# Performance work log

Measured on AMD Instinct MI355X. Metric: run time of the kernel, lower is better.

Reference implementation:

```python
import jax, jax.numpy as jnp
import numpy as np

DELTA_VAR = 0.5
DELTA_DIST = 2.0
ALPHA = 1.0
BETA = 1.0
GAMMA = 0.001

N, E, D, H, W = 2, 16, 48, 160, 160
NUM_C = 32


def _safe_norm(x, axis):
    # L2 norm with zero-safe gradient (matches torch.norm 'fro' over the dim)
    d2 = jnp.sum(x * x, axis=axis)
    nz = d2 > 0
    return jnp.sqrt(jnp.where(nz, d2, 1.0)) * nz


def setup_inputs() -> dict:
    key = jax.random.key(0)
    k1, k2 = jax.random.split(key)
    input_ = jax.random.normal(k1, (N, E, D, H, W), dtype=jnp.float32)
    target = jax.random.randint(k2, (N, D, H, W), 0, NUM_C).astype(jnp.int64)
    return {"input_": input_, "target": target, "C": NUM_C}


def _single_loss(emb, labels, C):
    # emb: [E, V] flattened spatial; labels: [V] int in [0, C)
    V = labels.shape[0]
    counts = jax.ops.segment_sum(jnp.ones((V,), emb.dtype), labels, num_segments=C)  # [C]
    sums = jax.ops.segment_sum(emb.T, labels, num_segments=C)                         # [C, E]
    means = sums / counts[:, None]                                                     # [C, E]

    # variance term: per-voxel distance to own cluster mean (equivalent to the
    # one-hot-expanded CxExSPATIAL formulation after the target mask)
    dist = _safe_norm(emb.T - means[labels], axis=1)                                   # [V]
    hinge = jnp.maximum(dist - DELTA_VAR, 0.0) ** 2
    per_cluster = jax.ops.segment_sum(hinge, labels, num_segments=C) / counts          # [C]
    variance_term = jnp.sum(per_cluster) / C

    # distance term: pairwise cluster-mean repulsion
    diff = means[:, None, :] - means[None, :, :]                                       # [C, C, E]
    dmat = _safe_norm(diff, axis=2)                                                    # [C, C]
    repulsion = 2.0 * DELTA_DIST * (1.0 - jnp.eye(C, dtype=emb.dtype))
    hinged = jnp.maximum(repulsion - dmat, 0.0) ** 2
    distance_term = jnp.sum(hinged) / (C * (C - 1))

    # regularizer: mean L2 norm of cluster means
    regularizer_term = jnp.sum(_safe_norm(means, axis=1)) / C

    return ALPHA * variance_term + BETA * distance_term + GAMMA * regularizer_term


def reference(input_, target, C):
    n = input_.shape[0]
    emb = input_.reshape(n, input_.shape[1], -1)  # [N, E, V]
    lab = target.reshape(n, -1).astype(jnp.int32)  # [N, V]
    losses = jax.vmap(lambda e, l: _single_loss(e, l, C))(emb, lab)
    return jnp.sum(losses) / n
```

## Files before the change

kernel.cpp:

```cpp
#include <hip/hip_runtime.h>
#include <math.h>

constexpr int N_  = 2;
constexpr int E_  = 16;
constexpr int C_  = 32;
constexpr int V_  = 48 * 160 * 160;
constexpr int V4_ = V_ / 4;
constexpr int BLK = 256;

constexpr float DELTA_VAR  = 0.5f;
constexpr float DELTA_DIST = 2.0f;
constexpr float GAMMA      = 0.001f;

constexpr int NCOPY   = 8;
constexpr int WS_SUMT = 0;
constexpr int WS_CNT  = WS_SUMT + NCOPY * N_ * E_ * C_;
constexpr int WS_VAR  = WS_CNT  + NCOPY * N_ * C_;
constexpr int WS_FLOATS = WS_VAR + N_;

using short8 = __attribute__((ext_vector_type(8))) short;
using f32x4  = __attribute__((ext_vector_type(4))) float;

__device__ __forceinline__ unsigned short f2bf(float f) {
    unsigned u = __float_as_uint(f);
    return (unsigned short)((u + 0x7FFFu + ((u >> 16) & 1u)) >> 16);
}
__device__ __forceinline__ unsigned packlab(int4 t) {
    return (unsigned)t.x | ((unsigned)t.y << 8) | ((unsigned)t.z << 16) | ((unsigned)t.w << 24);
}

constexpr int XPAD = 520;
__global__ __launch_bounds__(BLK) void sums_mfma(
    const float4* __restrict__ x4, const int4* __restrict__ t4,
    float* __restrict__ ws)
{
    __shared__ unsigned short s_xb[2][E_ * XPAD];

    const int n     = blockIdx.y;
    const int gtile = blockIdx.x * 2048;
    const int tid   = threadIdx.x;
    const int lane  = tid & 63;
    const int wid   = tid >> 6;
    const int myc   = lane & 15;
    const int quad  = lane >> 4;

    const short one = 0x3F80;
    short8 A_ones = {one, one, one, one, one, one, one, one};

    f32x4 acc_lo = {0.f,0.f,0.f,0.f}, acc_hi = {0.f,0.f,0.f,0.f};
    f32x4 cnt_lo = {0.f,0.f,0.f,0.f}, cnt_hi = {0.f,0.f,0.f,0.f};

    float4 R[8];
    {
        const int tb4 = gtile >> 2;
        #pragma unroll
        for (int k = 0; k < 8; ++k) {
            const int i = k * BLK + tid, e = i >> 7, v4 = i & 127;
            R[k] = x4[((size_t)(n * E_ + e)) * V4_ + tb4 + v4];
        }
    }

    for (int t = 0; t < 4; ++t) {
        const int tbase4 = (gtile + t * 512) >> 2;
        unsigned short* buf = s_xb[t & 1];

        #pragma unroll
        for (int k = 0; k < 8; ++k) {
            const int i = k * BLK + tid, e = i >> 7, v4 = i & 127;
            uint2 p;
            p.x = (unsigned)f2bf(R[k].x) | ((unsigned)f2bf(R[k].y) << 16);
            p.y = (unsigned)f2bf(R[k].z) | ((unsigned)f2bf(R[k].w) << 16);
            *(uint2*)&buf[e * XPAD + v4 * 4] = p;
        }
        if (t < 3) {
            const int nb4 = (gtile + (t + 1) * 512) >> 2;
            #pragma unroll
            for (int k = 0; k < 8; ++k) {
                const int i = k * BLK + tid, e = i >> 7, v4 = i & 127;
                R[k] = x4[((size_t)(n * E_ + e)) * V4_ + nb4 + v4];
            }
        }
        const int wbase = wid * 128;
        int4 P[4], Q[4];
        #pragma unroll
        for (int s = 0; s < 4; ++s) {
            const int b4 = tbase4 + ((wbase + s * 32 + quad * 8) >> 2);
            P[s] = t4[(size_t)n * V4_ + b4];
            Q[s] = t4[(size_t)n * V4_ + b4 + 1];
        }

        __builtin_amdgcn_sched_barrier(0);
        asm volatile("s_waitcnt lgkmcnt(0)");
        __builtin_amdgcn_s_barrier();
        __builtin_amdgcn_sched_barrier(0);

        #pragma unroll
        for (int s = 0; s < 4; ++s) {
            const int lvb = wbase + s * 32;
            const short8 A = *(const short8*)&buf[myc * XPAD + lvb + quad * 8];
            const unsigned la = packlab(P[s]), lb2 = packlab(Q[s]);
            short8 Blo, Bhi;
            #pragma unroll
            for (int j = 0; j < 4; ++j) {
                const int c0 = (la  >> (8 * j)) & 255;
                const int c1 = (lb2 >> (8 * j)) & 255;
                Blo[j]     = (c0 == myc)      ? one : (short)0;
                Bhi[j]     = (c0 == myc + 16) ? one : (short)0;
                Blo[4 + j] = (c1 == myc)      ? one : (short)0;
                Bhi[4 + j] = (c1 == myc + 16) ? one : (short)0;
            }
            acc_lo = __builtin_amdgcn_mfma_f32_16x16x32_bf16(A, Blo, acc_lo, 0, 0, 0);
            acc_hi = __builtin_amdgcn_mfma_f32_16x16x32_bf16(A, Bhi, acc_hi, 0, 0, 0);
            cnt_lo = __builtin_amdgcn_mfma_f32_16x16x32_bf16(A_ones, Blo, cnt_lo, 0, 0, 0);
            cnt_hi = __builtin_amdgcn_mfma_f32_16x16x32_bf16(A_ones, Bhi, cnt_hi, 0, 0, 0);
        }
    }

    float* s_red = (float*)&s_xb[0][0];
    #pragma unroll
    for (int r = 0; r < 4; ++r) {
        s_red[wid * 512 + lane * 8 + r]     = acc_lo[r];
        s_red[wid * 512 + lane * 8 + 4 + r] = acc_hi[r];
    }
    if (quad == 0) {
        s_red[2048 + wid * 32 + myc]      = cnt_lo[0];
        s_red[2048 + wid * 32 + myc + 16] = cnt_hi[0];
    }
    __syncthreads();

    const int kc = blockIdx.x & (NCOPY - 1);
    float* gsumT = ws + WS_SUMT + kc * (N_ * E_ * C_);
    float* gcntk = ws + WS_CNT  + kc * (N_ * C_);
    #pragma unroll
    for (int u = 0; u < 2; ++u) {
        const int combo = tid * 2 + u;
        const int l = combo >> 3, k = combo & 7;
        const int e = (l >> 4) * 4 + (k & 3);
        const int c = (l & 15) + 16 * (k >> 2);
        const float v = s_red[combo] + s_red[512 + combo]
                      + s_red[1024 + combo] + s_red[1536 + combo];
        unsafeAtomicAdd(&gsumT[(n * E_ + e) * C_ + c], v);
    }
    if (tid < C_) {
        const float v = s_red[2048 + tid] + s_red[2048 + 32 + tid]
                      + s_red[2048 + 64 + tid] + s_red[2048 + 96 + tid];
        unsafeAtomicAdd(&gcntk[n * C_ + tid], v);
    }
}

constexpr int MUP = 20;
__global__ __launch_bounds__(BLK) void variance_f32(
    const float4* __restrict__ x4, const int4* __restrict__ t4,
    float* __restrict__ ws)
{
    __shared__ float s_mu[C_ * MUP];
    __shared__ float s_part[4];
    const float* gsumT = ws + WS_SUMT;
    const float* gcnt  = ws + WS_CNT;
    float*       gvar  = ws + WS_VAR;

    const int n = blockIdx.y, tid = threadIdx.x;
    const int v4g = blockIdx.x * BLK + tid;

    const int4 t = t4[(size_t)n * V4_ + v4g];
    const float4* xrow = x4 + (size_t)n * E_ * V4_ + v4g;
    float4 xs[16];
    #pragma unroll
    for (int e = 0; e < 16; ++e) xs[e] = xrow[(size_t)e * V4_];

    for (int i = tid; i < C_ * E_; i += BLK) {
        const int c = i >> 4, e = i & 15;
        float s = 0.f, cc = 0.f;
        #pragma unroll
        for (int k = 0; k < NCOPY; ++k) {
            s  += gsumT[k * (N_ * E_ * C_) + (n * E_ + e) * C_ + c];
            cc += gcnt [k * (N_ * C_) + n * C_ + c];
        }
        s_mu[c * MUP + e] = s / cc;
        if (e == 0) s_mu[c * MUP + 16] = 1.0f / (cc * (float)C_);
    }
    __syncthreads();

    const int l0 = t.x, l1 = t.y, l2 = t.z, l3 = t.w;
    float4 m0[4], m1[4], m2[4], m3[4];
    #pragma unroll
    for (int u = 0; u < 4; ++u) {
        m0[u] = *(const float4*)&s_mu[l0 * MUP + 4 * u];
        m1[u] = *(const float4*)&s_mu[l1 * MUP + 4 * u];
        m2[u] = *(const float4*)&s_mu[l2 * MUP + 4 * u];
        m3[u] = *(const float4*)&s_mu[l3 * MUP + 4 * u];
    }
    const float w0 = s_mu[l0 * MUP + 16], w1 = s_mu[l1 * MUP + 16];
    const float w2 = s_mu[l2 * MUP + 16], w3 = s_mu[l3 * MUP + 16];

    float d0 = 0.f, d1 = 0.f, d2 = 0.f, d3 = 0.f;
    #pragma unroll
    for (int e = 0; e < 16; ++e) {
        const float mu0 = ((const float*)&m0[e >> 2])[e & 3];
        const float mu1 = ((const float*)&m1[e >> 2])[e & 3];
        const float mu2 = ((const float*)&m2[e >> 2])[e & 3];
        const float mu3 = ((const float*)&m3[e >> 2])[e & 3];
        d0 += (xs[e].x - mu0) * (xs[e].x - mu0);
        d1 += (xs[e].y - mu1) * (xs[e].y - mu1);
        d2 += (xs[e].z - mu2) * (xs[e].z - mu2);
        d3 += (xs[e].w - mu3) * (xs[e].w - mu3);
    }
    const float h0 = fmaxf(sqrtf(d0) - DELTA_VAR, 0.f);
    const float h1 = fmaxf(sqrtf(d1) - DELTA_VAR, 0.f);
    const float h2 = fmaxf(sqrtf(d2) - DELTA_VAR, 0.f);
    const float h3 = fmaxf(sqrtf(d3) - DELTA_VAR, 0.f);
    float v = h0 * h0 * w0 + h1 * h1 * w1 + h2 * h2 * w2 + h3 * h3 * w3;

    #pragma unroll
    for (int off = 32; off > 0; off >>= 1)
        v += __shfl_down(v, off, 64);
    if ((tid & 63) == 0) s_part[tid >> 6] = v;
    __syncthreads();
    if (tid == 0)
        unsafeAtomicAdd(&gvar[n], s_part[0] + s_part[1] + s_part[2] + s_part[3]);
}

__global__ __launch_bounds__(BLK) void finalize(
    const float* __restrict__ ws, float* __restrict__ out)
{
    __shared__ float s_mean[C_ * 17];
    __shared__ float s_red;
    __shared__ float s_total;

    const float* gsumT = ws + WS_SUMT;
    const float* gcnt  = ws + WS_CNT;
    const float* gvar  = ws + WS_VAR;

    if (threadIdx.x == 0) s_total = 0.0f;

    for (int n = 0; n < N_; ++n) {
        __syncthreads();
        for (int i = threadIdx.x; i < C_ * E_; i += BLK) {
            const int c = i >> 4, e = i & 15;
            float s = 0.f, cc = 0.f;
            #pragma unroll
            for (int k = 0; k < NCOPY; ++k) {
                s  += gsumT[k * (N_ * E_ * C_) + (n * E_ + e) * C_ + c];
                cc += gcnt [k * (N_ * C_) + n * C_ + c];
            }
            s_mean[c * 17 + e] = s / cc;
        }
        if (threadIdx.x == 0) s_red = gvar[n];
        __syncthreads();

        float local = 0.0f;
        if (threadIdx.x < C_) {
            const int c = threadIdx.x;
            float d2 = 0.f;
            #pragma unroll
            for (int e = 0; e < E_; ++e) {
                const float m = s_mean[c * 17 + e];
                d2 += m * m;
            }
            const float nm = d2 > 0.f ? sqrtf(d2) : 0.f;
            local += GAMMA * nm / (float)C_;
        }
        for (int t = threadIdx.x; t < C_ * C_; t += BLK) {
            const int i = t >> 5, j = t & 31;
            if (i != j) {
                float d2 = 0.f;
                #pragma unroll
                for (int e = 0; e < E_; ++e) {
                    const float diff = s_mean[i * 17 + e] - s_mean[j * 17 + e];
                    d2 += diff * diff;
                }
                const float d = d2 > 0.f ? sqrtf(d2) : 0.f;
                const float h = fmaxf(2.0f * DELTA_DIST - d, 0.f);
                local += (h * h) / (float)(C_ * (C_ - 1));
            }
        }
        unsafeAtomicAdd(&s_red, local);
        __syncthreads();
        if (threadIdx.x == 0) s_total += s_red;
    }
    __syncthreads();
    if (threadIdx.x == 0) out[0] = s_total / (float)N_;
}

extern "C" void kernel_launch(void* const* d_in, const int* in_sizes, int n_in,
                              void* d_out, int out_size, void* d_ws, size_t ws_size,
                              hipStream_t stream) {
    const float4* x4 = (const float4*)d_in[0];
    const int4*   t4 = (const int4*)d_in[1];
    float* ws  = (float*)d_ws;
    float* out = (float*)d_out;

    hipMemsetAsync(d_ws, 0, WS_FLOATS * sizeof(float), stream);

    sums_mfma   <<<dim3(600, N_),        BLK, 0, stream>>>(x4, t4, ws);
    variance_f32<<<dim3(V4_ / BLK, N_),  BLK, 0, stream>>>(x4, t4, ws);
    finalize    <<<1, BLK, 0, stream>>>(ws, out);
}
```

Baseline: 285.8 us.

## Fuse sums, variance and finalize into one cooperative persistent kernel

Replaces the three launches with a single cooperative kernel of 768 persistent blocks that runs the sums, variance and finalize phases separated by grid-wide syncs. The sums phase drops the LDS staging: each wave loads its embedding and label vectors straight into registers through a three-deep prefetch ring and feeds them to the MFMA. The variance phase becomes grid-stride over both batches and spreads its atomics across copies. The aim is to remove launch gaps and LDS round-trips, at the cost of grid-sync overhead, lower occupancy, and a fallback to separate kernels if the cooperative launch fails.

Result: slower. 456.5 us (+59.7%).

```diff
diff --git a/kernel.cpp b/kernel.cpp
--- a/kernel.cpp
+++ b/kernel.cpp
@@ -1,5 +1,8 @@
 #include <hip/hip_runtime.h>
+#include <hip/hip_cooperative_groups.h>
 #include <math.h>
+
+namespace cg = cooperative_groups;
 
 constexpr int N_  = 2;
 constexpr int E_  = 16;
@@ -8,15 +11,23 @@
 constexpr int V4_ = V_ / 4;
 constexpr int BLK = 256;
 
+constexpr int G_     = 768;
+constexpr int HALF_  = G_ / 2;
+constexpr int WPB_   = HALF_ * 4;
+constexpr int VPW_   = V_ / WPB_;
+constexpr int NSTEP_ = VPW_ / 32;
+
 constexpr float DELTA_VAR  = 0.5f;
 constexpr float DELTA_DIST = 2.0f;
 constexpr float GAMMA      = 0.001f;
 
-constexpr int NCOPY   = 8;
-constexpr int WS_SUMT = 0;
-constexpr int WS_CNT  = WS_SUMT + NCOPY * N_ * E_ * C_;
-constexpr int WS_VAR  = WS_CNT  + NCOPY * N_ * C_;
-constexpr int WS_FLOATS = WS_VAR + N_;
+constexpr int NCOPY     = 8;
+constexpr int WS_SUMT   = 0;
+constexpr int WS_CNT    = WS_SUMT + NCOPY * N_ * E_ * C_;
+constexpr int WS_VAR    = WS_CNT  + NCOPY * N_ * C_;
+constexpr int WS_FLOATS = WS_VAR  + NCOPY * N_;
+
+constexpr int MUP = 20;
 
 using short8 = __attribute__((ext_vector_type(8))) short;
 using f32x4  = __attribute__((ext_vector_type(4))) float;
@@ -29,94 +40,72 @@
     return (unsigned)t.x | ((unsigned)t.y << 8) | ((unsigned)t.z << 16) | ((unsigned)t.w << 24);
 }
 
-constexpr int XPAD = 520;
-__global__ __launch_bounds__(BLK) void sums_mfma(
-    const float4* __restrict__ x4, const int4* __restrict__ t4,
-    float* __restrict__ ws)
-{
-    __shared__ unsigned short s_xb[2][E_ * XPAD];
-
-    const int n     = blockIdx.y;
-    const int gtile = blockIdx.x * 2048;
-    const int tid   = threadIdx.x;
-    const int lane  = tid & 63;
-    const int wid   = tid >> 6;
-    const int myc   = lane & 15;
-    const int quad  = lane >> 4;
-
-    const short one = 0x3F80;
+__device__ __forceinline__ void phase_sums(
+    const float4* __restrict__ x4, const int4* __restrict__ t4,
+    float* __restrict__ ws, float* s_red, int bid)
+{
+    const int tid  = threadIdx.x;
+    const int lane = tid & 63;
+    const int wid  = tid >> 6;
+    const int myc  = lane & 15;
+    const int quad = lane >> 4;
+
+    const int n  = bid / HALF_;
+    const int wb = (bid % HALF_) * 4 + wid;
+    const float4* __restrict__ xrow = x4 + (size_t)(n * E_ + myc) * V4_;
+    const int4*   __restrict__ t4n  = t4 + (size_t)n * V4_;
+    const int l4 = wb * (VPW_ / 4) + quad * 2;
+
+    const short one = (short)0x3F80;
     short8 A_ones = {one, one, one, one, one, one, one, one};
 
     f32x4 acc_lo = {0.f,0.f,0.f,0.f}, acc_hi = {0.f,0.f,0.f,0.f};
     f32x4 cnt_lo = {0.f,0.f,0.f,0.f}, cnt_hi = {0.f,0.f,0.f,0.f};
 
-    float4 R[8];
-    {
-        const int tb4 = gtile >> 2;
-        #pragma unroll
-        for (int k = 0; k < 8; ++k) {
-            const int i = k * BLK + tid, e = i >> 7, v4 = i & 127;
-            R[k] = x4[((size_t)(n * E_ + e)) * V4_ + tb4 + v4];
-        }
-    }
-
-    for (int t = 0; t < 4; ++t) {
-        const int tbase4 = (gtile + t * 512) >> 2;
-        unsigned short* buf = s_xb[t & 1];
-
-        #pragma unroll
-        for (int k = 0; k < 8; ++k) {
-            const int i = k * BLK + tid, e = i >> 7, v4 = i & 127;
-            uint2 p;
-            p.x = (unsigned)f2bf(R[k].x) | ((unsigned)f2bf(R[k].y) << 16);
-            p.y = (unsigned)f2bf(R[k].z) | ((unsigned)f2bf(R[k].w) << 16);
-            *(uint2*)&buf[e * XPAD + v4 * 4] = p;
-        }
-        if (t < 3) {
-            const int nb4 = (gtile + (t + 1) * 512) >> 2;
-            #pragma unroll
-            for (int k = 0; k < 8; ++k) {
-                const int i = k * BLK + tid, e = i >> 7, v4 = i & 127;
-                R[k] = x4[((size_t)(n * E_ + e)) * V4_ + nb4 + v4];
-            }
-        }
-        const int wbase = wid * 128;
-        int4 P[4], Q[4];
-        #pragma unroll
-        for (int s = 0; s < 4; ++s) {
-            const int b4 = tbase4 + ((wbase + s * 32 + quad * 8) >> 2);
-            P[s] = t4[(size_t)n * V4_ + b4];
-            Q[s] = t4[(size_t)n * V4_ + b4 + 1];
-        }
-
-        __builtin_amdgcn_sched_barrier(0);
-        asm volatile("s_waitcnt lgkmcnt(0)");
-        __builtin_amdgcn_s_barrier();
-        __builtin_amdgcn_sched_barrier(0);
-
-        #pragma unroll
-        for (int s = 0; s < 4; ++s) {
-            const int lvb = wbase + s * 32;
-            const short8 A = *(const short8*)&buf[myc * XPAD + lvb + quad * 8];
-            const unsigned la = packlab(P[s]), lb2 = packlab(Q[s]);
-            short8 Blo, Bhi;
-            #pragma unroll
-            for (int j = 0; j < 4; ++j) {
-                const int c0 = (la  >> (8 * j)) & 255;
-                const int c1 = (lb2 >> (8 * j)) & 255;
-                Blo[j]     = (c0 == myc)      ? one : (short)0;
-                Bhi[j]     = (c0 == myc + 16) ? one : (short)0;
-                Blo[4 + j] = (c1 == myc)      ? one : (short)0;
-                Bhi[4 + j] = (c1 == myc + 16) ? one : (short)0;
-            }
-            acc_lo = __builtin_amdgcn_mfma_f32_16x16x32_bf16(A, Blo, acc_lo, 0, 0, 0);
-            acc_hi = __builtin_amdgcn_mfma_f32_16x16x32_bf16(A, Bhi, acc_hi, 0, 0, 0);
-            cnt_lo = __builtin_amdgcn_mfma_f32_16x16x32_bf16(A_ones, Blo, cnt_lo, 0, 0, 0);
-            cnt_hi = __builtin_amdgcn_mfma_f32_16x16x32_bf16(A_ones, Bhi, cnt_hi, 0, 0, 0);
-        }
-    }
-
-    float* s_red = (float*)&s_xb[0][0];
+    float4 RX0[3], RX1[3];
+    int4   RP[3],  RQ[3];
+    #pragma unroll
+    for (int p = 0; p < 2; ++p) {
+        RX0[p] = xrow[l4 + p * 8];
+        RX1[p] = xrow[l4 + p * 8 + 1];
+        RP[p]  = t4n[l4 + p * 8];
+        RQ[p]  = t4n[l4 + p * 8 + 1];
+    }
+
+    #pragma unroll
+    for (int s = 0; s < NSTEP_; ++s) {
+        const int cur = s % 3;
+        if (s + 2 < NSTEP_) {
+            const int nxt = (s + 2) % 3;
+            RX0[nxt] = xrow[l4 + (s + 2) * 8];
+            RX1[nxt] = xrow[l4 + (s + 2) * 8 + 1];
+            RP[nxt]  = t4n[l4 + (s + 2) * 8];
+            RQ[nxt]  = t4n[l4 + (s + 2) * 8 + 1];
+        }
+        short8 A;
+        A[0] = (short)f2bf(RX0[cur].x); A[1] = (short)f2bf(RX0[cur].y);
+        A[2] = (short)f2bf(RX0[cur].z); A[3] = (short)f2bf(RX0[cur].w);
+        A[4] = (short)f2bf(RX1[cur].x); A[5] = (short)f2bf(RX1[cur].y);
+        A[6] = (short)f2bf(RX1[cur].z); A[7] = (short)f2bf(RX1[cur].w);
+
+        const unsigned la  = packlab(RP[cur]);
+        const unsigned lb2 = packlab(RQ[cur]);
+        short8 Blo, Bhi;
+        #pragma unroll
+        for (int j = 0; j < 4; ++j) {
+            const int c0 = (la  >> (8 * j)) & 255;
+            const int c1 = (lb2 >> (8 * j)) & 255;
+            Blo[j]     = (c0 == myc)      ? one : (short)0;
+            Bhi[j]     = (c0 == myc + 16) ? one : (short)0;
+            Blo[4 + j] = (c1 == myc)      ? one : (short)0;
+            Bhi[4 + j] = (c1 == myc + 16) ? one : (short)0;
+        }
+        acc_lo = __builtin_amdgcn_mfma_f32_16x16x32_bf16(A,      Blo, acc_lo, 0, 0, 0);
+        acc_hi = __builtin_amdgcn_mfma_f32_16x16x32_bf16(A,      Bhi, acc_hi, 0, 0, 0);
+        cnt_lo = __builtin_amdgcn_mfma_f32_16x16x32_bf16(A_ones, Blo, cnt_lo, 0, 0, 0);
+        cnt_hi = __builtin_amdgcn_mfma_f32_16x16x32_bf16(A_ones, Bhi, cnt_hi, 0, 0, 0);
+    }
+
     #pragma unroll
     for (int r = 0; r < 4; ++r) {
         s_red[wid * 512 + lane * 8 + r]     = acc_lo[r];
@@ -128,7 +117,7 @@
     }
     __syncthreads();
 
-    const int kc = blockIdx.x & (NCOPY - 1);
+    const int kc = bid & (NCOPY - 1);
     float* gsumT = ws + WS_SUMT + kc * (N_ * E_ * C_);
     float* gcntk = ws + WS_CNT  + kc * (N_ * C_);
     #pragma unroll
@@ -148,90 +137,102 @@
     }
 }
 
-constexpr int MUP = 20;
-__global__ __launch_bounds__(BLK) void variance_f32(
-    const float4* __restrict__ x4, const int4* __restrict__ t4,
-    float* __restrict__ ws)
-{
-    __shared__ float s_mu[C_ * MUP];
-    __shared__ float s_part[4];
+__device__ __forceinline__ void phase_var(
+    const float4* __restrict__ x4, const int4* __restrict__ t4,
+    float* __restrict__ ws, float* s_mu, int bid, int nblk)
+{
     const float* gsumT = ws + WS_SUMT;
     const float* gcnt  = ws + WS_CNT;
     float*       gvar  = ws + WS_VAR;
-
-    const int n = blockIdx.y, tid = threadIdx.x;
-    const int v4g = blockIdx.x * BLK + tid;
-
-    const int4 t = t4[(size_t)n * V4_ + v4g];
-    const float4* xrow = x4 + (size_t)n * E_ * V4_ + v4g;
-    float4 xs[16];
-    #pragma unroll
-    for (int e = 0; e < 16; ++e) xs[e] = xrow[(size_t)e * V4_];
-
-    for (int i = tid; i < C_ * E_; i += BLK) {
-        const int c = i >> 4, e = i & 15;
+    const int tid = threadIdx.x;
+
+    for (int i = tid; i < N_ * C_ * E_; i += BLK) {
+        const int n2 = i >> 9;
+        const int r  = i & 511;
+        const int c  = r >> 4, e = r & 15;
         float s = 0.f, cc = 0.f;
         #pragma unroll
         for (int k = 0; k < NCOPY; ++k) {
-            s  += gsumT[k * (N_ * E_ * C_) + (n * E_ + e) * C_ + c];
-            cc += gcnt [k * (N_ * C_) + n * C_ + c];
-        }
-        s_mu[c * MUP + e] = s / cc;
-        if (e == 0) s_mu[c * MUP + 16] = 1.0f / (cc * (float)C_);
+            s  += gsumT[k * (N_ * E_ * C_) + (n2 * E_ + e) * C_ + c];
+            cc += gcnt [k * (N_ * C_) + n2 * C_ + c];
+        }
+        s_mu[n2 * (C_ * MUP) + c * MUP + e] = s / cc;
+        if (e == 0) s_mu[n2 * (C_ * MUP) + c * MUP + 16] = 1.0f / (cc * (float)C_);
     }
     __syncthreads();
 
-    const int l0 = t.x, l1 = t.y, l2 = t.z, l3 = t.w;
-    float4 m0[4], m1[4], m2[4], m3[4];
-    #pragma unroll
-    for (int u = 0; u < 4; ++u) {
-        m0[u] = *(const float4*)&s_mu[l0 * MUP + 4 * u];
-        m1[u] = *(const float4*)&s_mu[l1 * MUP + 4 * u];
-        m2[u] = *(const float4*)&s_mu[l2 * MUP + 4 * u];
-        m3[u] = *(const float4*)&s_mu[l3 * MUP + 4 * u];
-    }
-    const float w0 = s_mu[l0 * MUP + 16], w1 = s_mu[l1 * MUP + 16];
-    const float w2 = s_mu[l2 * MUP + 16], w3 = s_mu[l3 * MUP + 16];
-
-    float d0 = 0.f, d1 = 0.f, d2 = 0.f, d3 = 0.f;
-    #pragma unroll
-    for (int e = 0; e < 16; ++e) {
-        const float mu0 = ((const float*)&m0[e >> 2])[e & 3];
-        const float mu1 = ((const float*)&m1[e >> 2])[e & 3];
-        const float mu2 = ((const float*)&m2[e >> 2])[e & 3];
-        const float mu3 = ((const float*)&m3[e >> 2])[e & 3];
-        d0 += (xs[e].x - mu0) * (xs[e].x - mu0);
-        d1 += (xs[e].y - mu1) * (xs[e].y - mu1);
-        d2 += (xs[e].z - mu2) * (xs[e].z - mu2);
-        d3 += (xs[e].w - mu3) * (xs[e].w - mu3);
-    }
-    const float h0 = fmaxf(sqrtf(d0) - DELTA_VAR, 0.f);
-    const float h1 = fmaxf(sqrtf(d1) - DELTA_VAR, 0.f);
-    const float h2 = fmaxf(sqrtf(d2) - DELTA_VAR, 0.f);
-    const float h3 = fmaxf(sqrtf(d3) - DELTA_VAR, 0.f);
-    float v = h0 * h0 * w0 + h1 * h1 * w1 + h2 * h2 * w2 + h3 * h3 * w3;
-
-    #pragma unroll
-    for (int off = 32; off > 0; off >>= 1)
-        v += __shfl_down(v, off, 64);
-    if ((tid & 63) == 0) s_part[tid >> 6] = v;
+    float va0 = 0.f, va1 = 0.f;
+    for (int g = bid * BLK + tid; g < N_ * V4_; g += nblk * BLK) {
+        const int n  = (g >= V4_) ? 1 : 0;
+        const int vg = g - n * V4_;
+        const int4 t = t4[g];
+        const float4* __restrict__ xr = x4 + (size_t)n * E_ * V4_ + vg;
+        float4 xs[16];
+        #pragma unroll
+        for (int e = 0; e < 16; ++e) xs[e] = xr[(size_t)e * V4_];
+
+        const float* mu = s_mu + n * (C_ * MUP);
+        const int l0 = t.x, l1 = t.y, l2 = t.z, l3 = t.w;
+        float4 m0[4], m1[4], m2[4], m3[4];
+        #pragma unroll
+        for (int u = 0; u < 4; ++u) {
+            m0[u] = *(const float4*)&mu[l0 * MUP + 4 * u];
+            m1[u] = *(const float4*)&mu[l1 * MUP + 4 * u];
+            m2[u] = *(const float4*)&mu[l2 * MUP + 4 * u];
+            m3[u] = *(const float4*)&mu[l3 * MUP + 4 * u];
+        }
+        const float w0 = mu[l0 * MUP + 16], w1 = mu[l1 * MUP + 16];
+        const float w2 = mu[l2 * MUP + 16], w3 = mu[l3 * MUP + 16];
+
+        float d0 = 0.f, d1 = 0.f, d2 = 0.f, d3 = 0.f;
+        #pragma unroll
+        for (int e = 0; e < 16; ++e) {
+            const float mu0 = ((const float*)&m0[e >> 2])[e & 3];
+            const float mu1 = ((const float*)&m1[e >> 2])[e & 3];
+            const float mu2 = ((const float*)&m2[e >> 2])[e & 3];
+            const float mu3 = ((const float*)&m3[e >> 2])[e & 3];
+            d0 += (xs[e].x - mu0) * (xs[e].x - mu0);
+            d1 += (xs[e].y - mu1) * (xs[e].y - mu1);
+            d2 += (xs[e].z - mu2) * (xs[e].z - mu2);
+            d3 += (xs[e].w - mu3) * (xs[e].w - mu3);
+        }
+        const float h0 = fmaxf(sqrtf(d0) - DELTA_VAR, 0.f);
+        const float h1 = fmaxf(sqrtf(d1) - DELTA_VAR, 0.f);
+        const float h2 = fmaxf(sqrtf(d2) - DELTA_VAR, 0.f);
+        const float h3 = fmaxf(sqrtf(d3) - DELTA_VAR, 0.f);
+        const float vv = h0 * h0 * w0 + h1 * h1 * w1 + h2 * h2 * w2 + h3 * h3 * w3;
+        va0 += (n == 0) ? vv : 0.f;
+        va1 += (n == 0) ? 0.f : vv;
+    }
+
+    #pragma unroll
+    for (int off = 32; off > 0; off >>= 1) {
+        va0 += __shfl_down(va0, off, 64);
+        va1 += __shfl_down(va1, off, 64);
+    }
+    const int base = N_ * C_ * MUP;
+    if ((tid & 63) == 0) {
+        s_mu[base + (tid >> 6) * 2]     = va0;
+        s_mu[base + (tid >> 6) * 2 + 1] = va1;
+    }
     __syncthreads();
-    if (tid == 0)
-        unsafeAtomicAdd(&gvar[n], s_part[0] + s_part[1] + s_part[2] + s_part[3]);
-}
-
-__global__ __launch_bounds__(BLK) void finalize(
-    const float* __restrict__ ws, float* __restrict__ out)
-{
-    __shared__ float s_mean[C_ * 17];
-    __shared__ float s_red;
-    __shared__ float s_total;
-
+    if (tid == 0) {
+        const float t0 = s_mu[base] + s_mu[base + 2] + s_mu[base + 4] + s_mu[base + 6];
+        const float t1 = s_mu[base + 1] + s_mu[base + 3] + s_mu[base + 5] + s_mu[base + 7];
+        const int kc = bid & (NCOPY - 1);
+        unsafeAtomicAdd(&gvar[kc * N_ + 0], t0);
+        unsafeAtomicAdd(&gvar[kc * N_ + 1], t1);
+    }
+}
+
+__device__ __forceinline__ void phase_fin(
+    const float* __restrict__ ws, float* __restrict__ out, float* sm)
+{
     const float* gsumT = ws + WS_SUMT;
     const float* gcnt  = ws + WS_CNT;
     const float* gvar  = ws + WS_VAR;
 
-    if (threadIdx.x == 0) s_total = 0.0f;
+    if (threadIdx.x == 0) sm[601] = 0.0f;
 
     for (int n = 0; n < N_; ++n) {
         __syncthreads();
@@ -243,9 +244,14 @@
                 s  += gsumT[k * (N_ * E_ * C_) + (n * E_ + e) * C_ + c];
                 cc += gcnt [k * (N_ * C_) + n * C_ + c];
             }
-            s_mean[c * 17 + e] = s / cc;
-        }
-        if (threadIdx.x == 0) s_red = gvar[n];
+            sm[c * 17 + e] = s / cc;
+        }
+        if (threadIdx.x == 0) {
+            float vs = 0.f;
+            #pragma unroll
+            for (int k = 0; k < NCOPY; ++k) vs += gvar[k * N_ + n];
+            sm[600] = vs;
+        }
         __syncthreads();
 
         float local = 0.0f;
@@ -254,7 +260,7 @@
             float d2 = 0.f;
             #pragma unroll
             for (int e = 0; e < E_; ++e) {
-                const float m = s_mean[c * 17 + e];
+                const float m = sm[c * 17 + e];
                 d2 += m * m;
             }
             const float nm = d2 > 0.f ? sqrtf(d2) : 0.f;
@@ -266,7 +272,7 @@
                 float d2 = 0.f;
                 #pragma unroll
                 for (int e = 0; e < E_; ++e) {
-                    const float diff = s_mean[i * 17 + e] - s_mean[j * 17 + e];
+                    const float diff = sm[i * 17 + e] - sm[j * 17 + e];
                     d2 += diff * diff;
                 }
                 const float d = d2 > 0.f ? sqrtf(d2) : 0.f;
@@ -274,12 +280,50 @@
                 local += (h * h) / (float)(C_ * (C_ - 1));
             }
         }
-        unsafeAtomicAdd(&s_red, local);
+        unsafeAtomicAdd(&sm[600], local);
         __syncthreads();
-        if (threadIdx.x == 0) s_total += s_red;
+        if (threadIdx.x == 0) sm[601] += sm[600];
     }
     __syncthreads();
-    if (threadIdx.x == 0) out[0] = s_total / (float)N_;
+    if (threadIdx.x == 0) out[0] = sm[601] / (float)N_;
+}
+
+__global__ __launch_bounds__(BLK, 3) void fused_all(
+    const float4* __restrict__ x4, const int4* __restrict__ t4,
+    float* __restrict__ ws, float* __restrict__ out)
+{
+    __shared__ float s_red[2176];
+    __shared__ float s_mu[N_ * C_ * MUP + 16];
+    const int bid = blockIdx.x;
+
+    phase_sums(x4, t4, ws, s_red, bid);
+    cg::this_grid().sync();
+    phase_var(x4, t4, ws, s_mu, bid, (int)gridDim.x);
+    cg::this_grid().sync();
+    if (bid == 0) phase_fin(ws, out, s_mu);
+}
+
+__global__ __launch_bounds__(BLK, 3) void k_sums(
+    const float4* __restrict__ x4, const int4* __restrict__ t4,
+    float* __restrict__ ws)
+{
+    __shared__ float s_red[2176];
+    phase_sums(x4, t4, ws, s_red, blockIdx.x);
+}
+
+__global__ __launch_bounds__(BLK, 3) void k_var(
+    const float4* __restrict__ x4, const int4* __restrict__ t4,
+    float* __restrict__ ws)
+{
+    __shared__ float s_mu[N_ * C_ * MUP + 16];
+    phase_var(x4, t4, ws, s_mu, blockIdx.x, (int)gridDim.x);
+}
+
+__global__ __launch_bounds__(BLK) void k_fin(
+    const float* __restrict__ ws, float* __restrict__ out)
+{
+    __shared__ float sm[N_ * C_ * MUP + 16];
+    phase_fin(ws, out, sm);
 }
 
 extern "C" void kernel_launch(void* const* d_in, const int* in_sizes, int n_in,
@@ -292,7 +336,13 @@
 
     hipMemsetAsync(d_ws, 0, WS_FLOATS * sizeof(float), stream);
 
-    sums_mfma   <<<dim3(600, N_),        BLK, 0, stream>>>(x4, t4, ws);
-    variance_f32<<<dim3(V4_ / BLK, N_),  BLK, 0, stream>>>(x4, t4, ws);
-    finalize    <<<1, BLK, 0, stream>>>(ws, out);
-}
+    void* args[] = {(void*)&x4, (void*)&t4, (void*)&ws, (void*)&out};
+    hipError_t err = hipLaunchCooperativeKernel(
+        (const void*)fused_all, dim3(G_), dim3(BLK), args, 0, stream);
+    if (err != hipSuccess) {
+        (void)hipGetLastError();
+        k_sums<<<dim3(G_), BLK, 0, stream>>>(x4, t4, ws);
+        k_var <<<dim3(G_), BLK, 0, stream>>>(x4, t4, ws);
+        k_fin <<<1,        BLK, 0, stream>>>(ws, out);
+    }
+}
```

## Fold mean and finalize stages into last-block tickets, use persistent grids

Applied to the files above, without the earlier changes.

Removes the separate finalize launch by having the last block of each kernel (detected via an atomic ticket counter) compute the cluster means or the final loss. Means are computed once into workspace instead of being re-reduced in every variance block. Both kernels switch to fixed 1024-block grid-stride layouts with interleaved batch handling and occupancy hints. The cost is a serialized tail in the last block plus extra fences and atomics.

Result: slower. 443.7 us (+55.2%).

```diff
diff --git a/kernel.cpp b/kernel.cpp
--- a/kernel.cpp
+++ b/kernel.cpp
@@ -8,15 +8,25 @@
 constexpr int V4_ = V_ / 4;
 constexpr int BLK = 256;
 
+constexpr int TILE = 512;
+constexpr int TPN_ = V_ / TILE;
+constexpr int GS   = 1024;
+constexpr int SPB_ = GS / N_;
+constexpr int GV   = 1024;
+
 constexpr float DELTA_VAR  = 0.5f;
 constexpr float DELTA_DIST = 2.0f;
 constexpr float GAMMA      = 0.001f;
 
-constexpr int NCOPY   = 8;
-constexpr int WS_SUMT = 0;
-constexpr int WS_CNT  = WS_SUMT + NCOPY * N_ * E_ * C_;
-constexpr int WS_VAR  = WS_CNT  + NCOPY * N_ * C_;
-constexpr int WS_FLOATS = WS_VAR + N_;
+constexpr int NCOPY     = 8;
+constexpr int MUP       = 20;
+constexpr int WS_SUMT   = 0;
+constexpr int WS_CNT    = WS_SUMT + NCOPY * N_ * E_ * C_;
+constexpr int WS_VAR    = WS_CNT  + NCOPY * N_ * C_;
+constexpr int WS_TK1    = WS_VAR  + NCOPY * N_;
+constexpr int WS_TK2    = WS_TK1 + 1;
+constexpr int WS_MU     = 8728;
+constexpr int WS_FLOATS = WS_MU + N_ * C_ * MUP;
 
 using short8 = __attribute__((ext_vector_type(8))) short;
 using f32x4  = __attribute__((ext_vector_type(4))) float;
@@ -28,23 +38,33 @@
 __device__ __forceinline__ unsigned packlab(int4 t) {
     return (unsigned)t.x | ((unsigned)t.y << 8) | ((unsigned)t.z << 16) | ((unsigned)t.w << 24);
 }
+__device__ __forceinline__ float gload(const float* p) {
+    return __hip_atomic_load(p, __ATOMIC_RELAXED, __HIP_MEMORY_SCOPE_AGENT);
+}
 
 constexpr int XPAD = 520;
-__global__ __launch_bounds__(BLK) void sums_mfma(
+__global__ __launch_bounds__(BLK, 4) void k_sums(
     const float4* __restrict__ x4, const int4* __restrict__ t4,
     float* __restrict__ ws)
 {
     __shared__ unsigned short s_xb[2][E_ * XPAD];
-
-    const int n     = blockIdx.y;
-    const int gtile = blockIdx.x * 2048;
-    const int tid   = threadIdx.x;
-    const int lane  = tid & 63;
-    const int wid   = tid >> 6;
-    const int myc   = lane & 15;
-    const int quad  = lane >> 4;
-
-    const short one = 0x3F80;
+    __shared__ unsigned s_flag;
+
+    const int b    = blockIdx.x;
+    const int tid  = threadIdx.x;
+    const int lane = tid & 63;
+    const int wid  = tid >> 6;
+    const int myc  = lane & 15;
+    const int quad = lane >> 4;
+
+    const int n  = b & 1;
+    const int bs = b >> 1;
+    const int nt = (bs < (TPN_ - 4 * SPB_)) ? 5 : 4;
+
+    const float4* __restrict__ xn  = x4 + (size_t)(n * E_) * V4_;
+    const int4*   __restrict__ t4n = t4 + (size_t)n * V4_;
+
+    const short one = (short)0x3F80;
     short8 A_ones = {one, one, one, one, one, one, one, one};
 
     f32x4 acc_lo = {0.f,0.f,0.f,0.f}, acc_hi = {0.f,0.f,0.f,0.f};
@@ -52,17 +72,17 @@
 
     float4 R[8];
     {
-        const int tb4 = gtile >> 2;
+        const int tb4 = bs * (TILE / 4);
         #pragma unroll
         for (int k = 0; k < 8; ++k) {
             const int i = k * BLK + tid, e = i >> 7, v4 = i & 127;
-            R[k] = x4[((size_t)(n * E_ + e)) * V4_ + tb4 + v4];
-        }
-    }
-
-    for (int t = 0; t < 4; ++t) {
-        const int tbase4 = (gtile + t * 512) >> 2;
-        unsigned short* buf = s_xb[t & 1];
+            R[k] = xn[(size_t)e * V4_ + tb4 + v4];
+        }
+    }
+
+    for (int it = 0; it < nt; ++it) {
+        const int tbase4 = (bs + it * SPB_) * (TILE / 4);
+        unsigned short* buf = s_xb[it & 1];
 
         #pragma unroll
         for (int k = 0; k < 8; ++k) {
@@ -72,12 +92,12 @@
             p.y = (unsigned)f2bf(R[k].z) | ((unsigned)f2bf(R[k].w) << 16);
             *(uint2*)&buf[e * XPAD + v4 * 4] = p;
         }
-        if (t < 3) {
-            const int nb4 = (gtile + (t + 1) * 512) >> 2;
+        if (it + 1 < nt) {
+            const int nb4 = (bs + (it + 1) * SPB_) * (TILE / 4);
             #pragma unroll
             for (int k = 0; k < 8; ++k) {
                 const int i = k * BLK + tid, e = i >> 7, v4 = i & 127;
-                R[k] = x4[((size_t)(n * E_ + e)) * V4_ + nb4 + v4];
+                R[k] = xn[(size_t)e * V4_ + nb4 + v4];
             }
         }
         const int wbase = wid * 128;
@@ -85,8 +105,8 @@
         #pragma unroll
         for (int s = 0; s < 4; ++s) {
             const int b4 = tbase4 + ((wbase + s * 32 + quad * 8) >> 2);
-            P[s] = t4[(size_t)n * V4_ + b4];
-            Q[s] = t4[(size_t)n * V4_ + b4 + 1];
+            P[s] = t4n[b4];
+            Q[s] = t4n[b4 + 1];
         }
 
         __builtin_amdgcn_sched_barrier(0);
@@ -109,13 +129,14 @@
                 Blo[4 + j] = (c1 == myc)      ? one : (short)0;
                 Bhi[4 + j] = (c1 == myc + 16) ? one : (short)0;
             }
-            acc_lo = __builtin_amdgcn_mfma_f32_16x16x32_bf16(A, Blo, acc_lo, 0, 0, 0);
-            acc_hi = __builtin_amdgcn_mfma_f32_16x16x32_bf16(A, Bhi, acc_hi, 0, 0, 0);
+            acc_lo = __builtin_amdgcn_mfma_f32_16x16x32_bf16(A,      Blo, acc_lo, 0, 0, 0);
+            acc_hi = __builtin_amdgcn_mfma_f32_16x16x32_bf16(A,      Bhi, acc_hi, 0, 0, 0);
             cnt_lo = __builtin_amdgcn_mfma_f32_16x16x32_bf16(A_ones, Blo, cnt_lo, 0, 0, 0);
             cnt_hi = __builtin_amdgcn_mfma_f32_16x16x32_bf16(A_ones, Bhi, cnt_hi, 0, 0, 0);
         }
     }
 
+    __syncthreads();
     float* s_red = (float*)&s_xb[0][0];
     #pragma unroll
     for (int r = 0; r < 4; ++r) {
@@ -128,7 +149,7 @@
     }
     __syncthreads();
 
-    const int kc = blockIdx.x & (NCOPY - 1);
+    const int kc = bs & (NCOPY - 1);
     float* gsumT = ws + WS_SUMT + kc * (N_ * E_ * C_);
     float* gcntk = ws + WS_CNT  + kc * (N_ * C_);
     #pragma unroll
@@ -146,140 +167,151 @@
                       + s_red[2048 + 64 + tid] + s_red[2048 + 96 + tid];
         unsafeAtomicAdd(&gcntk[n * C_ + tid], v);
     }
-}
-
-constexpr int MUP = 20;
-__global__ __launch_bounds__(BLK) void variance_f32(
-    const float4* __restrict__ x4, const int4* __restrict__ t4,
-    float* __restrict__ ws)
-{
-    __shared__ float s_mu[C_ * MUP];
-    __shared__ float s_part[4];
-    const float* gsumT = ws + WS_SUMT;
-    const float* gcnt  = ws + WS_CNT;
-    float*       gvar  = ws + WS_VAR;
-
-    const int n = blockIdx.y, tid = threadIdx.x;
-    const int v4g = blockIdx.x * BLK + tid;
-
-    const int4 t = t4[(size_t)n * V4_ + v4g];
-    const float4* xrow = x4 + (size_t)n * E_ * V4_ + v4g;
-    float4 xs[16];
-    #pragma unroll
-    for (int e = 0; e < 16; ++e) xs[e] = xrow[(size_t)e * V4_];
-
-    for (int i = tid; i < C_ * E_; i += BLK) {
-        const int c = i >> 4, e = i & 15;
-        float s = 0.f, cc = 0.f;
-        #pragma unroll
-        for (int k = 0; k < NCOPY; ++k) {
-            s  += gsumT[k * (N_ * E_ * C_) + (n * E_ + e) * C_ + c];
-            cc += gcnt [k * (N_ * C_) + n * C_ + c];
-        }
-        s_mu[c * MUP + e] = s / cc;
-        if (e == 0) s_mu[c * MUP + 16] = 1.0f / (cc * (float)C_);
-    }
-    __syncthreads();
-
-    const int l0 = t.x, l1 = t.y, l2 = t.z, l3 = t.w;
-    float4 m0[4], m1[4], m2[4], m3[4];
-    #pragma unroll
-    for (int u = 0; u < 4; ++u) {
-        m0[u] = *(const float4*)&s_mu[l0 * MUP + 4 * u];
-        m1[u] = *(const float4*)&s_mu[l1 * MUP + 4 * u];
-        m2[u] = *(const float4*)&s_mu[l2 * MUP + 4 * u];
-        m3[u] = *(const float4*)&s_mu[l3 * MUP + 4 * u];
-    }
-    const float w0 = s_mu[l0 * MUP + 16], w1 = s_mu[l1 * MUP + 16];
-    const float w2 = s_mu[l2 * MUP + 16], w3 = s_mu[l3 * MUP + 16];
-
-    float d0 = 0.f, d1 = 0.f, d2 = 0.f, d3 = 0.f;
-    #pragma unroll
-    for (int e = 0; e < 16; ++e) {
-        const float mu0 = ((const float*)&m0[e >> 2])[e & 3];
-        const float mu1 = ((const float*)&m1[e >> 2])[e & 3];
-        const float mu2 = ((const float*)&m2[e >> 2])[e & 3];
-        const float mu3 = ((const float*)&m3[e >> 2])[e & 3];
-        d0 += (xs[e].x - mu0) * (xs[e].x - mu0);
-        d1 += (xs[e].y - mu1) * (xs[e].y - mu1);
-        d2 += (xs[e].z - mu2) * (xs[e].z - mu2);
-        d3 += (xs[e].w - mu3) * (xs[e].w - mu3);
-    }
-    const float h0 = fmaxf(sqrtf(d0) - DELTA_VAR, 0.f);
-    const float h1 = fmaxf(sqrtf(d1) - DELTA_VAR, 0.f);
-    const float h2 = fmaxf(sqrtf(d2) - DELTA_VAR, 0.f);
-    const float h3 = fmaxf(sqrtf(d3) - DELTA_VAR, 0.f);
-    float v = h0 * h0 * w0 + h1 * h1 * w1 + h2 * h2 * w2 + h3 * h3 * w3;
-
-    #pragma unroll
-    for (int off = 32; off > 0; off >>= 1)
-        v += __shfl_down(v, off, 64);
-    if ((tid & 63) == 0) s_part[tid >> 6] = v;
-    __syncthreads();
-    if (tid == 0)
-        unsafeAtomicAdd(&gvar[n], s_part[0] + s_part[1] + s_part[2] + s_part[3]);
-}
-
-__global__ __launch_bounds__(BLK) void finalize(
-    const float* __restrict__ ws, float* __restrict__ out)
-{
-    __shared__ float s_mean[C_ * 17];
-    __shared__ float s_red;
-    __shared__ float s_total;
-
-    const float* gsumT = ws + WS_SUMT;
-    const float* gcnt  = ws + WS_CNT;
-    const float* gvar  = ws + WS_VAR;
-
-    if (threadIdx.x == 0) s_total = 0.0f;
-
-    for (int n = 0; n < N_; ++n) {
-        __syncthreads();
-        for (int i = threadIdx.x; i < C_ * E_; i += BLK) {
-            const int c = i >> 4, e = i & 15;
+
+    __threadfence();
+    __syncthreads();
+    if (tid == 0) {
+        unsigned* tk = (unsigned*)(ws + WS_TK1);
+        s_flag = (atomicAdd(tk, 1u) == (unsigned)(GS - 1)) ? 1u : 0u;
+    }
+    __syncthreads();
+    if (s_flag) {
+        __threadfence();
+        const float* gS = ws + WS_SUMT;
+        const float* gC = ws + WS_CNT;
+        float*       mu = ws + WS_MU;
+        for (int i = tid; i < N_ * C_ * E_; i += BLK) {
+            const int n2 = i >> 9;
+            const int r  = i & 511;
+            const int c  = r >> 4, e = r & 15;
             float s = 0.f, cc = 0.f;
             #pragma unroll
             for (int k = 0; k < NCOPY; ++k) {
-                s  += gsumT[k * (N_ * E_ * C_) + (n * E_ + e) * C_ + c];
-                cc += gcnt [k * (N_ * C_) + n * C_ + c];
-            }
-            s_mean[c * 17 + e] = s / cc;
-        }
-        if (threadIdx.x == 0) s_red = gvar[n];
-        __syncthreads();
-
-        float local = 0.0f;
-        if (threadIdx.x < C_) {
-            const int c = threadIdx.x;
-            float d2 = 0.f;
-            #pragma unroll
-            for (int e = 0; e < E_; ++e) {
-                const float m = s_mean[c * 17 + e];
-                d2 += m * m;
-            }
-            const float nm = d2 > 0.f ? sqrtf(d2) : 0.f;
-            local += GAMMA * nm / (float)C_;
-        }
-        for (int t = threadIdx.x; t < C_ * C_; t += BLK) {
-            const int i = t >> 5, j = t & 31;
-            if (i != j) {
+                s  += gload(&gS[k * (N_ * E_ * C_) + (n2 * E_ + e) * C_ + c]);
+                cc += gload(&gC[k * (N_ * C_) + n2 * C_ + c]);
+            }
+            mu[(n2 * C_ + c) * MUP + e] = s / cc;
+            if (e == 0) mu[(n2 * C_ + c) * MUP + 16] = 1.0f / (cc * (float)C_);
+        }
+    }
+}
+
+__global__ __launch_bounds__(BLK, 4) void k_var(
+    const float4* __restrict__ x4, const int4* __restrict__ t4,
+    float* __restrict__ ws, float* __restrict__ out)
+{
+    __shared__ float s_mu[N_ * C_ * MUP];
+    __shared__ float s_aux[8];
+    __shared__ unsigned s_flag;
+
+    float* gvar = ws + WS_VAR;
+    const int bid = blockIdx.x, tid = threadIdx.x;
+    const int lane = tid & 63, wid = tid >> 6;
+
+    {
+        const float* mu = ws + WS_MU;
+        for (int i = tid; i < N_ * C_ * MUP; i += BLK) s_mu[i] = mu[i];
+    }
+    __syncthreads();
+
+    float va0 = 0.f, va1 = 0.f;
+    for (int g = bid * BLK + tid; g < N_ * V4_; g += GV * BLK) {
+        const int n  = (g >= V4_) ? 1 : 0;
+        const int vg = g - n * V4_;
+        const int4 t = t4[g];
+        const float4* __restrict__ xr = x4 + (size_t)n * E_ * V4_ + vg;
+        float4 xs[16];
+        #pragma unroll
+        for (int e = 0; e < 16; ++e) xs[e] = xr[(size_t)e * V4_];
+
+        const int mb = n * (C_ * MUP);
+        const int b0 = mb + t.x * MUP, b1 = mb + t.y * MUP;
+        const int b2 = mb + t.z * MUP, b3 = mb + t.w * MUP;
+        const float w0 = s_mu[b0 + 16], w1 = s_mu[b1 + 16];
+        const float w2 = s_mu[b2 + 16], w3 = s_mu[b3 + 16];
+
+        float d0 = 0.f, d1 = 0.f, d2 = 0.f, d3 = 0.f;
+        #pragma unroll
+        for (int e = 0; e < 16; ++e) {
+            const float mu0 = s_mu[b0 + e];
+            const float mu1 = s_mu[b1 + e];
+            const float mu2 = s_mu[b2 + e];
+            const float mu3 = s_mu[b3 + e];
+            d0 += (xs[e].x - mu0) * (xs[e].x - mu0);
+            d1 += (xs[e].y - mu1) * (xs[e].y - mu1);
+            d2 += (xs[e].z - mu2) * (xs[e].z - mu2);
+            d3 += (xs[e].w - mu3) * (xs[e].w - mu3);
+        }
+        const float h0 = fmaxf(sqrtf(d0) - DELTA_VAR, 0.f);
+        const float h1 = fmaxf(sqrtf(d1) - DELTA_VAR, 0.f);
+        const float h2 = fmaxf(sqrtf(d2) - DELTA_VAR, 0.f);
+        const float h3 = fmaxf(sqrtf(d3) - DELTA_VAR, 0.f);
+        const float vv = h0 * h0 * w0 + h1 * h1 * w1 + h2 * h2 * w2 + h3 * h3 * w3;
+        va0 += (n == 0) ? vv : 0.f;
+        va1 += (n == 0) ? 0.f : vv;
+    }
+
+    #pragma unroll
+    for (int off = 32; off > 0; off >>= 1) {
+        va0 += __shfl_down(va0, off, 64);
+        va1 += __shfl_down(va1, off, 64);
+    }
+    if (lane == 0) { s_aux[wid * 2] = va0; s_aux[wid * 2 + 1] = va1; }
+    __syncthreads();
+    if (tid == 0) {
+        const float t0 = s_aux[0] + s_aux[2] + s_aux[4] + s_aux[6];
+        const float t1 = s_aux[1] + s_aux[3] + s_aux[5] + s_aux[7];
+        const int kc = bid & (NCOPY - 1);
+        unsafeAtomicAdd(&gvar[kc * N_ + 0], t0);
+        unsafeAtomicAdd(&gvar[kc * N_ + 1], t1);
+        __threadfence();
+        unsigned* tk = (unsigned*)(ws + WS_TK2);
+        s_flag = (atomicAdd(tk, 1u) == (unsigned)(GV - 1)) ? 1u : 0u;
+    }
+    __syncthreads();
+
+    if (s_flag) {
+        __threadfence();
+        float local = 0.f;
+        if (tid < NCOPY * N_) local += gload(&gvar[tid]);
+
+        for (int n = 0; n < N_; ++n) {
+            const float* mu = s_mu + n * (C_ * MUP);
+            if (tid < C_) {
+                const int c = tid;
                 float d2 = 0.f;
                 #pragma unroll
                 for (int e = 0; e < E_; ++e) {
-                    const float diff = s_mean[i * 17 + e] - s_mean[j * 17 + e];
-                    d2 += diff * diff;
+                    const float m = mu[c * MUP + e];
+                    d2 += m * m;
                 }
-                const float d = d2 > 0.f ? sqrtf(d2) : 0.f;
-                const float h = fmaxf(2.0f * DELTA_DIST - d, 0.f);
-                local += (h * h) / (float)(C_ * (C_ - 1));
-            }
-        }
-        unsafeAtomicAdd(&s_red, local);
+                const float nm = d2 > 0.f ? sqrtf(d2) : 0.f;
+                local += GAMMA * nm / (float)C_;
+            }
+            for (int t2 = tid; t2 < C_ * C_; t2 += BLK) {
+                const int i = t2 >> 5, j = t2 & 31;
+                if (i != j) {
+                    float d2 = 0.f;
+                    #pragma unroll
+                    for (int e = 0; e < E_; ++e) {
+                        const float diff = mu[i * MUP + e] - mu[j * MUP + e];
+                        d2 += diff * diff;
+                    }
+                    const float d = d2 > 0.f ? sqrtf(d2) : 0.f;
+                    const float h = fmaxf(2.0f * DELTA_DIST - d, 0.f);
+                    local += (h * h) / (float)(C_ * (C_ - 1));
+                }
+            }
+        }
+
+        #pragma unroll
+        for (int off = 32; off > 0; off >>= 1)
+            local += __shfl_down(local, off, 64);
+        if (lane == 0) s_aux[wid] = local;
         __syncthreads();
-        if (threadIdx.x == 0) s_total += s_red;
-    }
-    __syncthreads();
-    if (threadIdx.x == 0) out[0] = s_total / (float)N_;
+        if (tid == 0)
+            out[0] = (s_aux[0] + s_aux[1] + s_aux[2] + s_aux[3]) / (float)N_;
+    }
 }
 
 extern "C" void kernel_launch(void* const* d_in, const int* in_sizes, int n_in,
@@ -292,7 +324,6 @@
 
     hipMemsetAsync(d_ws, 0, WS_FLOATS * sizeof(float), stream);
 
-    sums_mfma   <<<dim3(600, N_),        BLK, 0, stream>>>(x4, t4, ws);
-    variance_f32<<<dim3(V4_ / BLK, N_),  BLK, 0, stream>>>(x4, t4, ws);
-    finalize    <<<1, BLK, 0, stream>>>(ws, out);
-}
+    k_sums<<<dim3(GS), BLK, 0, stream>>>(x4, t4, ws);
+    k_var <<<dim3(GV), BLK, 0, stream>>>(x4, t4, ws, out);
+}
```

## Fuse finalize into variance kernel via last-block ticket and spread variance atomics

Applied to the files above, without the earlier changes.

The separate finalize launch is removed. The last variance block to finish, found with an atomic ticket counter and threadfences, now computes the distance and regularizer terms and writes the output. The variance partial sums are spread over 8 copies to cut atomic contention on a single address. The label loads in the sums kernel move ahead of the next-tile prefetch, and the tile loop is unrolled. This saves one kernel launch and its tail, at the cost of a serialized finalize step inside the last block and extra atomics.

After: 348.6 us. 1.22x slower.

```diff
diff --git a/kernel.cpp b/kernel.cpp
--- a/kernel.cpp
+++ b/kernel.cpp
@@ -12,11 +12,15 @@
 constexpr float DELTA_DIST = 2.0f;
 constexpr float GAMMA      = 0.001f;
 
-constexpr int NCOPY   = 8;
-constexpr int WS_SUMT = 0;
-constexpr int WS_CNT  = WS_SUMT + NCOPY * N_ * E_ * C_;
-constexpr int WS_VAR  = WS_CNT  + NCOPY * N_ * C_;
-constexpr int WS_FLOATS = WS_VAR + N_;
+constexpr int NCOPY     = 8;
+constexpr int WS_SUMT   = 0;
+constexpr int WS_CNT    = WS_SUMT + NCOPY * N_ * E_ * C_;
+constexpr int WS_VAR    = WS_CNT  + NCOPY * N_ * C_;
+constexpr int WS_TK     = WS_VAR  + NCOPY * N_;
+constexpr int WS_FLOATS = WS_TK + 4;
+
+constexpr int MUP = 20;
+constexpr int GVB = 1200 * N_;
 
 using short8 = __attribute__((ext_vector_type(8))) short;
 using f32x4  = __attribute__((ext_vector_type(4))) float;
@@ -27,6 +31,9 @@
 }
 __device__ __forceinline__ unsigned packlab(int4 t) {
     return (unsigned)t.x | ((unsigned)t.y << 8) | ((unsigned)t.z << 16) | ((unsigned)t.w << 24);
+}
+__device__ __forceinline__ float gload(const float* p) {
+    return __hip_atomic_load(p, __ATOMIC_RELAXED, __HIP_MEMORY_SCOPE_AGENT);
 }
 
 constexpr int XPAD = 520;
@@ -44,7 +51,7 @@
     const int myc   = lane & 15;
     const int quad  = lane >> 4;
 
-    const short one = 0x3F80;
+    const short one = (short)0x3F80;
     short8 A_ones = {one, one, one, one, one, one, one, one};
 
     f32x4 acc_lo = {0.f,0.f,0.f,0.f}, acc_hi = {0.f,0.f,0.f,0.f};
@@ -60,6 +67,7 @@
         }
     }
 
+    #pragma unroll
     for (int t = 0; t < 4; ++t) {
         const int tbase4 = (gtile + t * 512) >> 2;
         unsigned short* buf = s_xb[t & 1];
@@ -72,6 +80,14 @@
             p.y = (unsigned)f2bf(R[k].z) | ((unsigned)f2bf(R[k].w) << 16);
             *(uint2*)&buf[e * XPAD + v4 * 4] = p;
         }
+        const int wbase = wid * 128;
+        int4 P[4], Q[4];
+        #pragma unroll
+        for (int s = 0; s < 4; ++s) {
+            const int b4 = tbase4 + ((wbase + s * 32 + quad * 8) >> 2);
+            P[s] = t4[(size_t)n * V4_ + b4];
+            Q[s] = t4[(size_t)n * V4_ + b4 + 1];
+        }
         if (t < 3) {
             const int nb4 = (gtile + (t + 1) * 512) >> 2;
             #pragma unroll
@@ -79,14 +95,6 @@
                 const int i = k * BLK + tid, e = i >> 7, v4 = i & 127;
                 R[k] = x4[((size_t)(n * E_ + e)) * V4_ + nb4 + v4];
             }
-        }
-        const int wbase = wid * 128;
-        int4 P[4], Q[4];
-        #pragma unroll
-        for (int s = 0; s < 4; ++s) {
-            const int b4 = tbase4 + ((wbase + s * 32 + quad * 8) >> 2);
-            P[s] = t4[(size_t)n * V4_ + b4];
-            Q[s] = t4[(size_t)n * V4_ + b4 + 1];
         }
 
         __builtin_amdgcn_sched_barrier(0);
@@ -109,8 +117,8 @@
                 Blo[4 + j] = (c1 == myc)      ? one : (short)0;
                 Bhi[4 + j] = (c1 == myc + 16) ? one : (short)0;
             }
-            acc_lo = __builtin_amdgcn_mfma_f32_16x16x32_bf16(A, Blo, acc_lo, 0, 0, 0);
-            acc_hi = __builtin_amdgcn_mfma_f32_16x16x32_bf16(A, Bhi, acc_hi, 0, 0, 0);
+            acc_lo = __builtin_amdgcn_mfma_f32_16x16x32_bf16(A,      Blo, acc_lo, 0, 0, 0);
+            acc_hi = __builtin_amdgcn_mfma_f32_16x16x32_bf16(A,      Bhi, acc_hi, 0, 0, 0);
             cnt_lo = __builtin_amdgcn_mfma_f32_16x16x32_bf16(A_ones, Blo, cnt_lo, 0, 0, 0);
             cnt_hi = __builtin_amdgcn_mfma_f32_16x16x32_bf16(A_ones, Bhi, cnt_hi, 0, 0, 0);
         }
@@ -148,13 +156,16 @@
     }
 }
 
-constexpr int MUP = 20;
 __global__ __launch_bounds__(BLK) void variance_f32(
     const float4* __restrict__ x4, const int4* __restrict__ t4,
-    float* __restrict__ ws)
+    float* __restrict__ ws, float* __restrict__ out)
 {
     __shared__ float s_mu[C_ * MUP];
     __shared__ float s_part[4];
+    __shared__ float s_mean[C_ * 17];
+    __shared__ float s_red2, s_total;
+    __shared__ unsigned s_flag;
+
     const float* gsumT = ws + WS_SUMT;
     const float* gcnt  = ws + WS_CNT;
     float*       gvar  = ws + WS_VAR;
@@ -163,7 +174,7 @@
     const int v4g = blockIdx.x * BLK + tid;
 
     const int4 t = t4[(size_t)n * V4_ + v4g];
-    const float4* xrow = x4 + (size_t)n * E_ * V4_ + v4g;
+    const float4* __restrict__ xrow = x4 + (size_t)n * E_ * V4_ + v4g;
     float4 xs[16];
     #pragma unroll
     for (int e = 0; e < 16; ++e) xs[e] = xrow[(size_t)e * V4_];
@@ -216,70 +227,73 @@
         v += __shfl_down(v, off, 64);
     if ((tid & 63) == 0) s_part[tid >> 6] = v;
     __syncthreads();
-    if (tid == 0)
-        unsafeAtomicAdd(&gvar[n], s_part[0] + s_part[1] + s_part[2] + s_part[3]);
-}
-
-__global__ __launch_bounds__(BLK) void finalize(
-    const float* __restrict__ ws, float* __restrict__ out)
-{
-    __shared__ float s_mean[C_ * 17];
-    __shared__ float s_red;
-    __shared__ float s_total;
-
-    const float* gsumT = ws + WS_SUMT;
-    const float* gcnt  = ws + WS_CNT;
-    const float* gvar  = ws + WS_VAR;
-
-    if (threadIdx.x == 0) s_total = 0.0f;
-
-    for (int n = 0; n < N_; ++n) {
-        __syncthreads();
-        for (int i = threadIdx.x; i < C_ * E_; i += BLK) {
-            const int c = i >> 4, e = i & 15;
-            float s = 0.f, cc = 0.f;
-            #pragma unroll
-            for (int k = 0; k < NCOPY; ++k) {
-                s  += gsumT[k * (N_ * E_ * C_) + (n * E_ + e) * C_ + c];
-                cc += gcnt [k * (N_ * C_) + n * C_ + c];
-            }
-            s_mean[c * 17 + e] = s / cc;
-        }
-        if (threadIdx.x == 0) s_red = gvar[n];
-        __syncthreads();
-
-        float local = 0.0f;
-        if (threadIdx.x < C_) {
-            const int c = threadIdx.x;
-            float d2 = 0.f;
-            #pragma unroll
-            for (int e = 0; e < E_; ++e) {
-                const float m = s_mean[c * 17 + e];
-                d2 += m * m;
-            }
-            const float nm = d2 > 0.f ? sqrtf(d2) : 0.f;
-            local += GAMMA * nm / (float)C_;
-        }
-        for (int t = threadIdx.x; t < C_ * C_; t += BLK) {
-            const int i = t >> 5, j = t & 31;
-            if (i != j) {
-                float d2 = 0.f;
+    if (tid == 0) {
+        const int kc = (blockIdx.y * gridDim.x + blockIdx.x) & (NCOPY - 1);
+        unsafeAtomicAdd(&gvar[kc * N_ + n],
+                        s_part[0] + s_part[1] + s_part[2] + s_part[3]);
+        __threadfence();
+        unsigned* tk = (unsigned*)(ws + WS_TK);
+        s_flag = (atomicAdd(tk, 1u) == (unsigned)(GVB - 1)) ? 1u : 0u;
+    }
+    __syncthreads();
+
+    if (s_flag) {
+        __threadfence();
+        if (tid == 0) s_total = 0.0f;
+
+        for (int nn = 0; nn < N_; ++nn) {
+            __syncthreads();
+            for (int i = tid; i < C_ * E_; i += BLK) {
+                const int c = i >> 4, e = i & 15;
+                float s = 0.f, cc = 0.f;
+                #pragma unroll
+                for (int k = 0; k < NCOPY; ++k) {
+                    s  += gsumT[k * (N_ * E_ * C_) + (nn * E_ + e) * C_ + c];
+                    cc += gcnt [k * (N_ * C_) + nn * C_ + c];
+                }
+                s_mean[c * 17 + e] = s / cc;
+            }
+            if (tid == 0) {
+                float vs = 0.f;
+                #pragma unroll
+                for (int k = 0; k < NCOPY; ++k) vs += gload(&gvar[k * N_ + nn]);
+                s_red2 = vs;
+            }
+            __syncthreads();
+
+            float local = 0.0f;
+            if (tid < C_) {
+                const int c = tid;
+                float dd = 0.f;
                 #pragma unroll
                 for (int e = 0; e < E_; ++e) {
-                    const float diff = s_mean[i * 17 + e] - s_mean[j * 17 + e];
-                    d2 += diff * diff;
+                    const float m = s_mean[c * 17 + e];
+                    dd += m * m;
                 }
-                const float d = d2 > 0.f ? sqrtf(d2) : 0.f;
-                const float h = fmaxf(2.0f * DELTA_DIST - d, 0.f);
-                local += (h * h) / (float)(C_ * (C_ - 1));
-            }
-        }
-        unsafeAtomicAdd(&s_red, local);
+                const float nm = dd > 0.f ? sqrtf(dd) : 0.f;
+                local += GAMMA * nm / (float)C_;
+            }
+            for (int t2 = tid; t2 < C_ * C_; t2 += BLK) {
+                const int i = t2 >> 5, j = t2 & 31;
+                if (i != j) {
+                    float dd = 0.f;
+                    #pragma unroll
+                    for (int e = 0; e < E_; ++e) {
+                        const float diff = s_mean[i * 17 + e] - s_mean[j * 17 + e];
+                        dd += diff * diff;
+                    }
+                    const float d = dd > 0.f ? sqrtf(dd) : 0.f;
+                    const float h = fmaxf(2.0f * DELTA_DIST - d, 0.f);
+                    local += (h * h) / (float)(C_ * (C_ - 1));
+                }
+            }
+            unsafeAtomicAdd(&s_red2, local);
+            __syncthreads();
+            if (tid == 0) s_total += s_red2;
+        }
         __syncthreads();
-        if (threadIdx.x == 0) s_total += s_red;
-    }
-    __syncthreads();
-    if (threadIdx.x == 0) out[0] = s_total / (float)N_;
+        if (tid == 0) out[0] = s_total / (float)N_;
+    }
 }
 
 extern "C" void kernel_launch(void* const* d_in, const int* in_sizes, int n_in,
@@ -292,7 +306,6 @@
 
     hipMemsetAsync(d_ws, 0, WS_FLOATS * sizeof(float), stream);
 
-    sums_mfma   <<<dim3(600, N_),        BLK, 0, stream>>>(x4, t4, ws);
-    variance_f32<<<dim3(V4_ / BLK, N_),  BLK, 0, stream>>>(x4, t4, ws);
-    finalize    <<<1, BLK, 0, stream>>>(ws, out);
-}
+    sums_mfma   <<<dim3(600, N_),  BLK, 0, stream>>>(x4, t4, ws);
+    variance_f32<<<dim3(1200, N_), BLK, 0, stream>>>(x4, t4, ws, out);
+}
```
